# Kernel tuning notes

Hardware: AMD Instinct MI355X
Metric: run time of the kernel (lower is better)

The kernel has to match this reference:

```python
import jax, jax.numpy as jnp
import numpy as np

D_MODEL = 512
N_HEADS = 8
D_K = D_MODEL // N_HEADS


def setup_inputs() -> dict:
    key = jax.random.key(0)
    ks = jax.random.split(key, 12)
    B, S = 2, 4096
    std = 1.0 / np.sqrt(D_MODEL)
    inp = {
        "q": jax.random.normal(ks[0], (B, S, D_MODEL), jnp.float32),
        "k": jax.random.normal(ks[1], (B, S, D_MODEL), jnp.float32),
        "v": jax.random.normal(ks[2], (B, S, D_MODEL), jnp.float32),
        "Wq": jax.random.normal(ks[3], (D_MODEL, D_MODEL), jnp.float32) * std,
        "bq": jnp.zeros((D_MODEL,), jnp.float32),
        "Wk": jax.random.normal(ks[4], (D_MODEL, D_MODEL), jnp.float32) * std,
        "bk": jnp.zeros((D_MODEL,), jnp.float32),
        "Wv": jax.random.normal(ks[5], (D_MODEL, D_MODEL), jnp.float32) * std,
        "bv": jnp.zeros((D_MODEL,), jnp.float32),
        "Wo": jax.random.normal(ks[6], (D_MODEL, D_MODEL), jnp.float32) * std,
        "bo": jnp.zeros((D_MODEL,), jnp.float32),
        # torch init: ones
        "time_decay": jnp.ones((1, N_HEADS, 1, 1), jnp.float32) * 0.01,
        "scale": jnp.ones((1,), jnp.float32),
    }
    return inp


def reference(q, k, v, Wq, bq, Wk, bk, Wv, bv, Wo, bo, time_decay, scale):
    B, S, _ = q.shape
    # projections (torch Linear: x @ W.T + b), reshape to [B, H, S, d_k]
    def proj(x, W, b):
        y = x @ W.T + b
        return y.reshape(B, -1, N_HEADS, D_K).transpose(0, 2, 1, 3)

    qh = proj(q, Wq, bq)
    kh = proj(k, Wk, bk)
    vh = proj(v, Wv, bv)

    # scores: [B, H, Sq, Sk]
    scores = jnp.einsum("bhqd,bhkd->bhqk", qh, kh) / np.sqrt(D_K)
    scores = scores * scale
    # exponential decay over absolute key position (per-head learnable rate)
    pos = jnp.arange(S, dtype=scores.dtype)  # key positions
    decay = jnp.exp(-time_decay * jnp.abs(pos)[None, None, None, :])  # [1,H,1,Sk]
    scores = scores * decay

    attn = jax.nn.softmax(scores, axis=-1)
    context = jnp.einsum("bhqk,bhkd->bhqd", attn, vh)
    context = context.transpose(0, 2, 1, 3).reshape(B, S, D_MODEL)
    out = context @ Wo.T + bo
    return out
```

## Files before the change

kernel.cpp:

```cpp
#include <hip/hip_runtime.h>
#include <hip/hip_bf16.h>
#include <stdint.h>

typedef __attribute__((ext_vector_type(8))) __bf16 bf16x8;
typedef __attribute__((ext_vector_type(4))) float f32x4;
typedef __attribute__((ext_vector_type(16))) float f32x16;
typedef __attribute__((ext_vector_type(8))) unsigned short ushort8;
typedef __attribute__((ext_vector_type(4))) unsigned short ushort4v;
typedef __attribute__((ext_vector_type(2))) unsigned int uint2v;
typedef __attribute__((ext_vector_type(4))) unsigned int uint4v;

__device__ __forceinline__ unsigned short bfbits(float x) {
    __bf16 b = (__bf16)x;
    return __builtin_bit_cast(unsigned short, b);
}
__device__ __forceinline__ float bf2f_u(unsigned short u) {
    return __builtin_bit_cast(float, (unsigned int)u << 16);
}

__device__ __forceinline__ f32x4 mfma16(bf16x8 a, bf16x8 b, f32x4 c) {
    return __builtin_amdgcn_mfma_f32_16x16x32_bf16(a, b, c, 0, 0, 0);
}
__device__ __forceinline__ f32x16 mfma32(bf16x8 a, bf16x8 b, f32x16 c) {
    return __builtin_amdgcn_mfma_f32_32x32x16_bf16(a, b, c, 0, 0, 0);
}

__device__ __forceinline__ unsigned int cvtpk(float lo, float hi) {
    unsigned int r;
    asm("v_cvt_pk_bf16_f32 %0, %1, %2" : "=v"(r) : "v"(lo), "v"(hi));
    return r;
}

__device__ __forceinline__ float lanepull(float src, int srcl) {
    return __builtin_bit_cast(float,
        __builtin_amdgcn_ds_bpermute(srcl * 4, __builtin_bit_cast(int, src)));
}

__device__ __forceinline__ void gload16(const void* g, void* l) {
    __builtin_amdgcn_global_load_lds(
        (const __attribute__((address_space(1))) unsigned int*)g,
        (__attribute__((address_space(3))) unsigned int*)l, 16, 0, 0);
}

__device__ __forceinline__ f32x16 zero16() {
    f32x16 r;
    #pragma unroll
    for (int i = 0; i < 16; i++) r[i] = 0.f;
    return r;
}

__device__ __forceinline__ int tail_tiles(float tdh, float scale) {
    float cut = 5.3f + __logf(fmaxf(scale, 1e-20f));
    cut = fmaxf(cut, 0.f);
    tdh = fmaxf(tdh, 1e-8f);
    int kt = (int)ceilf(cut / (tdh * 64.f));
    if (kt < 1) kt = 1;
    if (kt > 64) kt = 64;
    return kt;
}

__global__ __launch_bounds__(256) void wconv(
    const float* __restrict__ Wq, const float* __restrict__ Wk,
    const float* __restrict__ Wv, const float* __restrict__ Wo,
    unsigned short* __restrict__ Wbf)
{
    const int t    = blockIdx.x * 256 + threadIdx.x;
    const int slab = t >> 15;
    const int off8 = t & 32767;
    const float* src = (slab == 0) ? Wq : (slab == 1) ? Wk : (slab == 2) ? Wv : Wo;
    float4 a = ((const float4*)(src + off8 * 8))[0];
    float4 b = ((const float4*)(src + off8 * 8))[1];
    uint4v pk = { cvtpk(a.x, a.y), cvtpk(a.z, a.w), cvtpk(b.x, b.y), cvtpk(b.z, b.w) };
    *(uint4v*)(Wbf + (size_t)slab * 262144 + off8 * 8) = pk;
}

__global__ __launch_bounds__(256) void gemm_qkv(
    const float* __restrict__ q, const float* __restrict__ k, const float* __restrict__ v,
    const unsigned short* __restrict__ Wbf,
    const float* __restrict__ bq, const float* __restrict__ bk, const float* __restrict__ bv,
    const float* __restrict__ td, const float* __restrict__ sc,
    unsigned short* __restrict__ Qh, unsigned short* __restrict__ Kh,
    unsigned short* __restrict__ Vt)
{
    __shared__ __align__(16) char ALDS[2][16384];

    const int id  = blockIdx.x;
    const int nid = (id & 7) * 96 + (id >> 3);
    const int z   = nid >> 8;
    const int rem = nid & 255;
    const int bm  = rem >> 2;
    const int bn  = rem & 3;

    const float* A0   = (z == 0) ? q  : (z == 1) ? k  : v;
    const float* bias = (z == 0) ? bq : (z == 1) ? bk : bv;

    const int tid  = threadIdx.x;
    const int lane = tid & 63;
    const int w    = tid >> 6;
    const int wm   = w >> 1, wn = w & 1;
    const int l15  = lane & 15;
    const int g    = lane >> 4;

    const int lr  = lane >> 3;
    const int lc  = ((lane & 7) * 16) ^ (lr << 4);
    const char* asrc[4];
    #pragma unroll
    for (int j = 0; j < 4; j++)
        asrc[j] = (const char*)A0 + (size_t)(bm * 128 + w * 32 + j * 8 + lr) * 2048 + lc;
    int adst[4];
    #pragma unroll
    for (int j = 0; j < 4; j++) adst[j] = w * 4096 + j * 1024;

    const unsigned short* Bp[4];
    #pragma unroll
    for (int n = 0; n < 4; n++)
        Bp[n] = Wbf + (size_t)z * 262144
              + (size_t)(bn * 128 + wn * 64 + n * 16 + l15) * 512 + g * 8;

    f32x4 acc[4][4];
    #pragma unroll
    for (int m = 0; m < 4; m++)
        #pragma unroll
        for (int n = 0; n < 4; n++)
            acc[m][n] = (f32x4){0.f, 0.f, 0.f, 0.f};

    const int arow = l15;
    const int asw  = (arow & 7) << 4;

    #pragma unroll
    for (int j = 0; j < 4; j++) gload16(asrc[j], ALDS[0] + adst[j]);
    bf16x8 BA[4], BB[4];
    #pragma unroll
    for (int n = 0; n < 4; n++) BA[n] = *(const bf16x8*)Bp[n];

#define QKV_ITER(CUR, KK, BC, BN)                                                  \
    {                                                                              \
        asm volatile("s_waitcnt vmcnt(0)" ::: "memory");                           \
        __syncthreads();                                                           \
        if ((KK) < 15) {                                                           \
            _Pragma("unroll")                                                      \
            for (int j = 0; j < 4; j++)                                            \
                gload16(asrc[j] + (size_t)((KK) + 1) * 128,                        \
                        ALDS[(CUR) ^ 1] + adst[j]);                                \
            _Pragma("unroll")                                                      \
            for (int n = 0; n < 4; n++)                                            \
                BN[n] = *(const bf16x8*)(Bp[n] + (size_t)((KK) + 1) * 32);         \
        }                                                                          \
        bf16x8 af[4];                                                              \
        _Pragma("unroll")                                                          \
        for (int m = 0; m < 4; m++) {                                              \
            const char* base = ALDS[CUR] + (wm * 64 + m * 16 + arow) * 128;        \
            f32x4 v0 = *(const f32x4*)(base + ((g * 32) ^ asw));                   \
            f32x4 v1 = *(const f32x4*)(base + (((g * 32) | 16) ^ asw));            \
            uint4v pk = { cvtpk(v0.x, v0.y), cvtpk(v0.z, v0.w),                    \
                          cvtpk(v1.x, v1.y), cvtpk(v1.z, v1.w) };                  \
            af[m] = __builtin_bit_cast(bf16x8, pk);                                \
        }                                                                          \
        __builtin_amdgcn_s_setprio(1);                                             \
        _Pragma("unroll")                                                          \
        for (int m = 0; m < 4; m++)                                                \
            _Pragma("unroll")                                                      \
            for (int n = 0; n < 4; n++)                                            \
                acc[m][n] = mfma16(af[m], BC[n], acc[m][n]);                       \
        __builtin_amdgcn_s_setprio(0);                                             \
    }

    #pragma unroll 1
    for (int t = 0; t < 8; ++t) {
        QKV_ITER(0, 2 * t, BA, BB)
        QKV_ITER(1, 2 * t + 1, BB, BA)
    }
#undef QKV_ITER

    const float coefL = sc[0] * 0.125f * 1.44269504f;

    #pragma unroll
    for (int m = 0; m < 4; m++) {
        const int grow0 = bm * 128 + wm * 64 + m * 16 + (g << 2);
        #pragma unroll
        for (int n = 0; n < 4; n++) {
            const int gcol = bn * 128 + wn * 64 + n * 16 + l15;
            const float bv2 = bias[gcol];
            f32x4 c = acc[m][n];
            const int b = grow0 >> 12, s0 = grow0 & 4095;
            const int h = gcol >> 6, dk = gcol & 63;
            if (z == 0) {
                const size_t base = ((size_t)(b * 8 + h) * 4096 + s0) * 64 + dk;
                #pragma unroll
                for (int r = 0; r < 4; r++)
                    Qh[base + (size_t)r * 64] = bfbits((c[r] + bv2) * coefL);
            } else if (z == 1) {
                const float tdh = td[h];
                const size_t base = ((size_t)(b * 8 + h) * 4096 + s0) * 64 + dk;
                #pragma unroll
                for (int r = 0; r < 4; r++)
                    Kh[base + (size_t)r * 64] = bfbits((c[r] + bv2) * __expf(-tdh * (float)(s0 + r)));
            } else {
                ushort4v pk = { bfbits(c[0] + bv2), bfbits(c[1] + bv2),
                                bfbits(c[2] + bv2), bfbits(c[3] + bv2) };
                *(ushort4v*)&Vt[((size_t)(b * 8 + h) * 64 + dk) * 4096 + s0] = pk;
            }
        }
    }
}

__global__ __launch_bounds__(256) void gemm_out(
    const unsigned short* __restrict__ Actx, const unsigned short* __restrict__ Wob,
    const float* __restrict__ bias, float* __restrict__ Out)
{
    __shared__ __align__(16) char ALDS[2][16384];

    const int id  = blockIdx.x;
    const int nid = (id & 7) * 64 + (id >> 3);
    const int bm  = nid >> 3;
    const int bn  = nid & 7;

    const int tid  = threadIdx.x;
    const int lane = tid & 63;
    const int w    = tid >> 6;
    const int wm   = w >> 1, wn = w & 1;
    const int l15  = lane & 15;
    const int g    = lane >> 4;

    const int lr  = lane >> 3;
    const int lc  = ((lane & 7) * 16) ^ (lr << 4);
    const char* asrc[4];
    #pragma unroll
    for (int j = 0; j < 4; j++)
        asrc[j] = (const char*)Actx + (size_t)(bm * 128 + w * 32 + j * 8 + lr) * 1024 + lc;
    int adst[4];
    #pragma unroll
    for (int j = 0; j < 4; j++) adst[j] = w * 4096 + j * 1024;

    const unsigned short* Bp[2];
    #pragma unroll
    for (int n = 0; n < 2; n++)
        Bp[n] = Wob + (size_t)(bn * 64 + wn * 32 + n * 16 + l15) * 512 + g * 8;

    f32x4 acc[4][2];
    #pragma unroll
    for (int m = 0; m < 4; m++)
        #pragma unroll
        for (int n = 0; n < 2; n++)
            acc[m][n] = (f32x4){0.f, 0.f, 0.f, 0.f};

    const int arow = l15;
    const int asw  = (arow & 7) << 4;

    #pragma unroll
    for (int j = 0; j < 4; j++) gload16(asrc[j], ALDS[0] + adst[j]);
    bf16x8 BA[2][2], BB[2][2];
    #pragma unroll
    for (int n = 0; n < 2; n++) {
        BA[n][0] = *(const bf16x8*)Bp[n];
        BA[n][1] = *(const bf16x8*)(Bp[n] + 32);
    }

#define OUT_ITER(CUR, KK, BC, BN)                                                  \
    {                                                                              \
        asm volatile("s_waitcnt vmcnt(0)" ::: "memory");                           \
        __syncthreads();                                                           \
        if ((KK) < 7) {                                                            \
            _Pragma("unroll")                                                      \
            for (int j = 0; j < 4; j++)                                            \
                gload16(asrc[j] + (size_t)((KK) + 1) * 128,                        \
                        ALDS[(CUR) ^ 1] + adst[j]);                                \
            _Pragma("unroll")                                                      \
            for (int n = 0; n < 2; n++) {                                          \
                BN[n][0] = *(const bf16x8*)(Bp[n] + (size_t)((KK) + 1) * 64);      \
                BN[n][1] = *(const bf16x8*)(Bp[n] + (size_t)((KK) + 1) * 64 + 32); \
            }                                                                      \
        }                                                                          \
        bf16x8 af[4][2];                                                           \
        _Pragma("unroll")                                                          \
        for (int m = 0; m < 4; m++) {                                              \
            const char* base = ALDS[CUR] + (wm * 64 + m * 16 + arow) * 128;        \
            af[m][0] = *(const bf16x8*)(base + ((g * 16) ^ asw));                  \
            af[m][1] = *(const bf16x8*)(base + ((64 + g * 16) ^ asw));             \
        }                                                                          \
        __builtin_amdgcn_s_setprio(1);                                             \
        _Pragma("unroll")                                                          \
        for (int m = 0; m < 4; m++)                                                \
            _Pragma("unroll")                                                      \
            for (int n = 0; n < 2; n++) {                                          \
                acc[m][n] = mfma16(af[m][0], BC[n][0], acc[m][n]);                 \
                acc[m][n] = mfma16(af[m][1], BC[n][1], acc[m][n]);                 \
            }                                                                      \
        __builtin_amdgcn_s_setprio(0);                                             \
    }

    #pragma unroll 1
    for (int t = 0; t < 4; ++t) {
        OUT_ITER(0, 2 * t, BA, BB)
        OUT_ITER(1, 2 * t + 1, BB, BA)
    }
#undef OUT_ITER

    #pragma unroll
    for (int m = 0; m < 4; m++) {
        const int grow0 = bm * 128 + wm * 64 + m * 16 + (g << 2);
        #pragma unroll
        for (int n = 0; n < 2; n++) {
            const int gcol = bn * 64 + wn * 32 + n * 16 + l15;
            const float bv2 = bias[gcol];
            f32x4 c = acc[m][n];
            #pragma unroll
            for (int r = 0; r < 4; r++)
                Out[(size_t)(grow0 + r) * 512 + gcol] = c[r] + bv2;
        }
    }
}

__global__ __launch_bounds__(512) void tail_pre(
    const unsigned short* __restrict__ Kh, const unsigned short* __restrict__ Vt,
    const float* __restrict__ td, const float* __restrict__ sc,
    unsigned short* __restrict__ Mt, float* __restrict__ SumV, float* __restrict__ KsL)
{
    __shared__ __align__(16) char KLDS[2][8192];
    __shared__ float redM[4][32][32];
    __shared__ float redv[64];
    __shared__ float redk[64];

    const int blk  = blockIdx.x;
    const int bh   = blk >> 3;
    const int part = blk & 7;
    const int h    = bh & 7;
    const int tid  = threadIdx.x;
    const int w    = tid >> 6;
    const int lane = tid & 63;
    const int l31  = lane & 31, hl = lane >> 5;
    const int d2q  = w & 1, d1q = (w >> 1) & 1, ksub = w >> 2;

    const int KT   = tail_tiles(td[h], sc[0]);
    const int K0   = KT * 64;
    const int nk   = 4096 - K0;
    const int q64  = nk >> 6;
    const int qb   = q64 >> 3, qr = q64 & 7;
    const int nch  = qb + (part < qr ? 1 : 0);
    const int ch0  = part * qb + (part < qr ? part : qr);
    const int kbeg = K0 + ch0 * 64;

    const int lr = lane >> 3;
    const int r8 = (w * 8 + lr) & 7;
    const char* ksrc = (const char*)Kh + (size_t)(bh * 4096 + kbeg + w * 8 + lr) * 128
                     + (((lane & 7) * 16) ^ (r8 << 4));
    const int kdst = w * 1024;

    const unsigned short* Vp = Vt + (size_t)(bh * 64 + d2q * 32 + l31) * 4096 + kbeg;

    f32x16 macc = zero16();
    float sumv = 0.f, ksum = 0.f;

    if (nch > 0) gload16(ksrc, KLDS[0] + kdst);

    #pragma unroll 1
    for (int ch = 0; ch < nch; ++ch) {
        asm volatile("s_waitcnt vmcnt(0)" ::: "memory");
        __syncthreads();
        if (ch + 1 < nch)
            gload16(ksrc + (size_t)(ch + 1) * 8192, KLDS[(ch + 1) & 1] + kdst);
        const char* kb = KLDS[ch & 1];

        #pragma unroll
        for (int mf = 0; mf < 2; mf++) {
            const int kloc0 = ksub * 32 + mf * 16 + hl * 8;
            ushort8 kbv;
            #pragma unroll
            for (int e = 0; e < 8; e++) {
                const int row = kloc0 + e;
                kbv[e] = *(const unsigned short*)(kb + row * 128
                          + ((d1q * 64 + l31 * 2) ^ ((row & 7) << 4)));
            }
            if (d2q == 0) {
                #pragma unroll
                for (int e = 0; e < 8; e++) ksum += bf2f_u(kbv[e]);
            }
            bf16x8 av = *(const bf16x8*)(Vp + ch * 64 + kloc0);
            if (d1q == 0) {
                ushort8 au = __builtin_bit_cast(ushort8, av);
                #pragma unroll
                for (int e = 0; e < 8; e++) sumv += bf2f_u(au[e]);
            }
            macc = mfma32(av, __builtin_bit_cast(bf16x8, kbv), macc);
        }
    }

    sumv += __shfl_xor(sumv, 32);
    ksum += __shfl_xor(ksum, 32);

    const int quad = d2q * 2 + d1q;
    __syncthreads();
    if (ksub == 0) {
        #pragma unroll
        for (int r = 0; r < 16; r++) {
            const int row = (r & 3) + 8 * (r >> 2) + 4 * hl;
            redM[quad][row][l31] = macc[r];
        }
        if (d1q == 0 && hl == 0) redv[d2q * 32 + l31] = sumv;
        if (d2q == 0 && hl == 0) redk[d1q * 32 + l31] = ksum;
    }
    __syncthreads();
    if (ksub == 1) {
        unsigned short* Mb = Mt + (size_t)part * 16 * 4096 + (size_t)bh * 4096;
        #pragma unroll
        for (int r = 0; r < 16; r++) {
            const int row = (r & 3) + 8 * (r >> 2) + 4 * hl;
            const float mv = (macc[r] + redM[quad][row][l31]) * 0.6931472f;
            Mb[(size_t)(d2q * 32 + row) * 64 + d1q * 32 + l31] = bfbits(mv);
        }
        if (d1q == 0 && hl == 0)
            SumV[part * 1024 + bh * 64 + d2q * 32 + l31] = sumv + redv[d2q * 32 + l31];
        if (d2q == 0 && hl == 0)
            KsL[part * 1024 + bh * 64 + d1q * 32 + l31] = (ksum + redk[d1q * 32 + l31]) * 0.6931472f;
    }
}

__global__ __launch_bounds__(256, 4) void attn_decay(
    const unsigned short* __restrict__ Qh, const unsigned short* __restrict__ Kh,
    const unsigned short* __restrict__ Vt, const float* __restrict__ td,
    const float* __restrict__ sc,
    const unsigned short* __restrict__ Mt, const float* __restrict__ SumV,
    const float* __restrict__ KsL, unsigned short* __restrict__ ctx)
{
    __shared__ __align__(16) char LDSB[32768];

    const int tid  = threadIdx.x;
    const int lane = tid & 63;
    const int w    = tid >> 6;
    const int qg   = w >> 1;
    const int ws   = w & 1;
    const int l31  = lane & 31;
    const int hl   = lane >> 5;

    const int i  = blockIdx.x;
    const int bh = ((i & 7) << 1) | ((i >> 9) & 1);
    const int qt = (i >> 3) & 63;
    const int h  = bh & 7;
    const int b  = bh >> 3;

    const int KT = tail_tiles(td[h], sc[0]);
    const int nk = 4096 - KT * 64;

    bf16x8 qf[4];
    {
        const unsigned short* Qp =
            Qh + ((size_t)bh * 4096 + qt * 64 + qg * 32 + l31) * 64 + hl * 8;
        #pragma unroll
        for (int c = 0; c < 4; c++)
            qf[c] = *(const bf16x8*)(Qp + c * 16);
    }

    f32x16 o0 = zero16(), o1 = zero16();
    float lp = 0.f;

    const char* kgp0; const char* kgp1; const char* vgp0; const char* vgp1;
    int ldsoff0, ldsoff1;
    {
        const size_t kbaseB = (size_t)bh * 4096 * 64 * 2;
        const size_t vbaseB = (size_t)bh * 64 * 4096 * 2;
        const int p0 = w * 2048 + lane * 16;
        const int r0 = p0 >> 7, c0 = p0 & 127, sw0 = (r0 & 7) << 4;
        const int p1 = w * 2048 + 1024 + lane * 16;
        const int r1 = p1 >> 7, c1 = p1 & 127, sw1 = (r1 & 7) << 4;
        kgp0 = (const char*)Kh + kbaseB + (size_t)r0 * 128  + (c0 ^ sw0);
        kgp1 = (const char*)Kh + kbaseB + (size_t)r1 * 128  + (c1 ^ sw1);
        vgp0 = (const char*)Vt + vbaseB + (size_t)r0 * 8192 + (c0 ^ sw0);
        vgp1 = (const char*)Vt + vbaseB + (size_t)r1 * 8192 + (c1 ^ sw1);
        ldsoff0 = w * 2048;
        ldsoff1 = w * 2048 + 1024;
    }
    gload16(kgp0, LDSB + ldsoff0);
    gload16(kgp1, LDSB + ldsoff1);
    gload16(vgp0, LDSB + 16384 + ldsoff0);
    gload16(vgp1, LDSB + 16384 + ldsoff1);
    kgp0 += 8192; kgp1 += 8192; vgp0 += 128; vgp1 += 128;

    const int krow = ws * 32 + l31;
    const int ksw  = (krow & 7) << 4;

#define ATTN_TILE(CUR, KT_IDX)                                                    \
    {                                                                             \
        asm volatile("s_waitcnt vmcnt(0)" ::: "memory");                          \
        __syncthreads();                                                          \
        if ((KT_IDX) + 1 < KT) {                                                  \
            gload16(kgp0, LDSB + ((CUR) ^ 1) * 8192 + ldsoff0);                   \
            gload16(kgp1, LDSB + ((CUR) ^ 1) * 8192 + ldsoff1);                   \
            gload16(vgp0, LDSB + 16384 + ((CUR) ^ 1) * 8192 + ldsoff0);           \
            gload16(vgp1, LDSB + 16384 + ((CUR) ^ 1) * 8192 + ldsoff1);           \
            kgp0 += 8192; kgp1 += 8192; vgp0 += 128; vgp1 += 128;                 \
        }                                                                         \
        const char* kb = LDSB + (CUR) * 8192;                                     \
        const char* vb = LDSB + 16384 + (CUR) * 8192;                             \
        f32x16 s = zero16();                                                      \
        __builtin_amdgcn_s_setprio(1);                                            \
        _Pragma("unroll")                                                         \
        for (int c = 0; c < 4; c++) {                                             \
            bf16x8 kf = *(const bf16x8*)(kb + krow * 128 + ((c * 32 + hl * 16) ^ ksw)); \
            s = mfma32(kf, qf[c], s);                                             \
        }                                                                         \
        __builtin_amdgcn_s_setprio(0);                                            \
        float p[16];                                                              \
        _Pragma("unroll")                                                         \
        for (int r = 0; r < 16; r++) {                                            \
            p[r] = __builtin_amdgcn_exp2f(s[r]);                                  \
            lp += p[r];                                                           \
        }                                                                         \
        unsigned int W0 = cvtpk(p[0], p[1]),   W1 = cvtpk(p[2], p[3]);            \
        unsigned int W2 = cvtpk(p[4], p[5]),   W3 = cvtpk(p[6], p[7]);            \
        unsigned int W4 = cvtpk(p[8], p[9]),   W5 = cvtpk(p[10], p[11]);          \
        unsigned int W6 = cvtpk(p[12], p[13]), W7 = cvtpk(p[14], p[15]);          \
        uint2v r02 = __builtin_amdgcn_permlane32_swap(W0, W2, false, false);      \
        uint2v r13 = __builtin_amdgcn_permlane32_swap(W1, W3, false, false);      \
        uint2v r46 = __builtin_amdgcn_permlane32_swap(W4, W6, false, false);      \
        uint2v r57 = __builtin_amdgcn_permlane32_swap(W5, W7, false, false);      \
        bf16x8 pa0 = __builtin_bit_cast(bf16x8, (uint4v){r02.x, r13.x, r02.y, r13.y}); \
        bf16x8 pa1 = __builtin_bit_cast(bf16x8, (uint4v){r46.x, r57.x, r46.y, r57.y}); \
        __builtin_amdgcn_s_setprio(1);                                            \
        {                                                                         \
            const int vr0  = l31;                                                 \
            const int vsw0 = (vr0 & 7) << 4;                                      \
            bf16x8 va = *(const bf16x8*)(vb + vr0 * 128 + ((ws * 64 + hl * 16) ^ vsw0));      \
            bf16x8 vb2 = *(const bf16x8*)(vb + vr0 * 128 + ((ws * 64 + 32 + hl * 16) ^ vsw0));\
            o0 = mfma32(pa0, va, o0);                                             \
            o0 = mfma32(pa1, vb2, o0);                                            \
            const int vr1  = 32 + l31;                                            \
            const int vsw1 = (vr1 & 7) << 4;                                      \
            bf16x8 vc = *(const bf16x8*)(vb + vr1 * 128 + ((ws * 64 + hl * 16) ^ vsw1));      \
            bf16x8 vd = *(const bf16x8*)(vb + vr1 * 128 + ((ws * 64 + 32 + hl * 16) ^ vsw1)); \
            o1 = mfma32(pa0, vc, o1);                                             \
            o1 = mfma32(pa1, vd, o1);                                             \
        }                                                                         \
        __builtin_amdgcn_s_setprio(0);                                            \
    }

    const int KT2 = KT >> 1;
    #pragma unroll 1
    for (int t = 0; t < KT2; ++t) {
        ATTN_TILE(0, 2 * t)
        ATTN_TILE(1, 2 * t + 1)
    }
    if (KT & 1) {
        ATTN_TILE(0, KT - 1)
    }
#undef ATTN_TILE

    if (ws == 0 && nk > 0) {
        float qk = 0.f;
        #pragma unroll
        for (int c = 0; c < 4; c++) {
            ushort8 qb2 = __builtin_bit_cast(ushort8, qf[c]);
            #pragma unroll
            for (int e = 0; e < 8; e++) {
                const int idx = c * 16 + hl * 8 + e;
                float ks = 0.f;
                #pragma unroll
                for (int part = 0; part < 8; part++)
                    ks += KsL[part * 1024 + bh * 64 + idx];
                qk += bf2f_u(qb2[e]) * ks;
            }
        }
        qk += __shfl_xor(qk, 32);
        if (hl == 0) lp += (float)nk + qk;

        #pragma unroll 1
        for (int part = 0; part < 8; part++) {
            const unsigned short* Mb = Mt + (size_t)part * 16 * 4096 + (size_t)bh * 4096;
            #pragma unroll
            for (int c = 0; c < 4; c++) {
                bf16x8 m0 = *(const bf16x8*)(Mb + (size_t)l31 * 64 + c * 16 + hl * 8);
                bf16x8 m1 = *(const bf16x8*)(Mb + (size_t)(32 + l31) * 64 + c * 16 + hl * 8);
                o0 = mfma32(qf[c], m0, o0);
                o1 = mfma32(qf[c], m1, o1);
            }
        }
        float sv0 = 0.f, sv1 = 0.f;
        #pragma unroll
        for (int part = 0; part < 8; part++) {
            sv0 += SumV[part * 1024 + bh * 64 + l31];
            sv1 += SumV[part * 1024 + bh * 64 + 32 + l31];
        }
        #pragma unroll
        for (int r = 0; r < 16; r++) { o0[r] += sv0; o1[r] += sv1; }
    }

    float lw = lp + __shfl_xor(lp, 32);
    __syncthreads();
    float* lscr = (float*)(LDSB + 16384);
    if (lane < 32)
        lscr[(qg * 2 + ws) * 32 + lane] = lw;
    __syncthreads();
    const float pl2 = lscr[(qg * 2 + (ws ^ 1)) * 32 + l31];
    const float myscale = 1.f / (lw + pl2);
    #pragma unroll
    for (int rc = 0; rc < 4; rc++)
        #pragma unroll
        for (int j = 0; j < 4; j++) {
            const float a = lanepull(myscale, rc * 8 + hl * 4 + j);
            o0[rc * 4 + j] *= a;
            o1[rc * 4 + j] *= a;
        }
    __syncthreads();
    float* Oscr = (float*)(LDSB + qg * 8192);
    if (ws == 1) {
        #pragma unroll
        for (int reg = 0; reg < 16; reg++) {
            const int row = (reg & 3) + 8 * (reg >> 2) + 4 * hl;
            Oscr[row * 64 + l31]      = o0[reg];
            Oscr[row * 64 + 32 + l31] = o1[reg];
        }
    }
    __syncthreads();
    if (ws == 0) {
        #pragma unroll
        for (int reg = 0; reg < 16; reg++) {
            const int row = (reg & 3) + 8 * (reg >> 2) + 4 * hl;
            const float v0 = o0[reg] + Oscr[row * 64 + l31];
            const float v1 = o1[reg] + Oscr[row * 64 + 32 + l31];
            const int srow_ = qt * 64 + qg * 32 + row;
            const size_t idx = ((size_t)b * 4096 + srow_) * 512 + h * 64;
            ctx[idx + l31]      = bfbits(v0);
            ctx[idx + 32 + l31] = bfbits(v1);
        }
    }
}

extern "C" void kernel_launch(void* const* d_in, const int* in_sizes, int n_in,
                              void* d_out, int out_size, void* d_ws, size_t ws_size,
                              hipStream_t stream)
{
    (void)in_sizes; (void)n_in; (void)out_size; (void)ws_size;
    const float* q  = (const float*)d_in[0];
    const float* k  = (const float*)d_in[1];
    const float* v  = (const float*)d_in[2];
    const float* Wq = (const float*)d_in[3];
    const float* bq = (const float*)d_in[4];
    const float* Wk = (const float*)d_in[5];
    const float* bk = (const float*)d_in[6];
    const float* Wv = (const float*)d_in[7];
    const float* bv = (const float*)d_in[8];
    const float* Wo = (const float*)d_in[9];
    const float* bo = (const float*)d_in[10];
    const float* td = (const float*)d_in[11];
    const float* sc = (const float*)d_in[12];

    unsigned short* Qh  = (unsigned short*)d_ws;
    unsigned short* Kh  = Qh + (size_t)16 * 4096 * 64;
    unsigned short* Vt  = Kh + (size_t)16 * 4096 * 64;
    unsigned short* ctx = Vt + (size_t)16 * 4096 * 64;
    unsigned short* Wbf = ctx + (size_t)16 * 4096 * 64;

    unsigned short* Mt   = (unsigned short*)d_out;
    float*          SumV = (float*)((char*)d_out + 8 * 16 * 4096 * 2);
    float*          KsL  = SumV + 8 * 1024;

    wconv<<<dim3(512), 256, 0, stream>>>(Wq, Wk, Wv, Wo, Wbf);
    gemm_qkv<<<dim3(768), 256, 0, stream>>>(q, k, v, Wbf, bq, bk, bv, td, sc, Qh, Kh, Vt);
    tail_pre<<<dim3(128), 512, 0, stream>>>(Kh, Vt, td, sc, Mt, SumV, KsL);
    attn_decay<<<dim3(1024), 256, 0, stream>>>(Qh, Kh, Vt, td, sc, Mt, SumV, KsL, ctx);
    gemm_out<<<dim3(512), 256, 0, stream>>>(ctx, Wbf + (size_t)3 * 262144, bo, (float*)d_out);
}
```

Baseline: 115.9 us.

## Triple-buffer QKV GEMM loads with partial vmcnt waits

The QKV projection GEMM moves from double to triple buffering of the A tile in LDS and B fragments in registers, prefetching two k-steps ahead. It waits with vmcnt(8) instead of draining all outstanding loads, and the loop is fully unrolled. This aims to hide global load latency behind MFMA work. The cost is 48KB of LDS, which may lower occupancy, plus more register pressure. Correctness depends on the vmcnt count matching the number of loads in flight.

Measured after the change: 114.0 us. Within noise of the previous version (-1.7%).

```diff
diff --git a/kernel.cpp b/kernel.cpp
--- a/kernel.cpp
+++ b/kernel.cpp
@@ -82,7 +82,7 @@
     unsigned short* __restrict__ Qh, unsigned short* __restrict__ Kh,
     unsigned short* __restrict__ Vt)
 {
-    __shared__ __align__(16) char ALDS[2][16384];
+    __shared__ __align__(16) char ALDS[3][16384];
 
     const int id  = blockIdx.x;
     const int nid = (id & 7) * 96 + (id >> 3);
@@ -127,29 +127,36 @@
     const int arow = l15;
     const int asw  = (arow & 7) << 4;
 
+    bf16x8 B0[4], B1[4], B2[4];
+
     #pragma unroll
     for (int j = 0; j < 4; j++) gload16(asrc[j], ALDS[0] + adst[j]);
-    bf16x8 BA[4], BB[4];
-    #pragma unroll
-    for (int n = 0; n < 4; n++) BA[n] = *(const bf16x8*)Bp[n];
-
-#define QKV_ITER(CUR, KK, BC, BN)                                                  \
+    #pragma unroll
+    for (int n = 0; n < 4; n++) B0[n] = *(const bf16x8*)Bp[n];
+    #pragma unroll
+    for (int j = 0; j < 4; j++) gload16(asrc[j] + 128, ALDS[1] + adst[j]);
+    #pragma unroll
+    for (int n = 0; n < 4; n++) B1[n] = *(const bf16x8*)(Bp[n] + 32);
+
+#define QKV_ITER(KK, BC, BN)                                                       \
     {                                                                              \
-        asm volatile("s_waitcnt vmcnt(0)" ::: "memory");                           \
-        __syncthreads();                                                           \
-        if ((KK) < 15) {                                                           \
+        if ((KK) == 15) { asm volatile("s_waitcnt vmcnt(0)" ::: "memory"); }       \
+        else            { asm volatile("s_waitcnt vmcnt(8)" ::: "memory"); }       \
+        __builtin_amdgcn_s_barrier();                                              \
+        __builtin_amdgcn_sched_barrier(0);                                         \
+        if ((KK) + 2 < 16) {                                                       \
             _Pragma("unroll")                                                      \
             for (int j = 0; j < 4; j++)                                            \
-                gload16(asrc[j] + (size_t)((KK) + 1) * 128,                        \
-                        ALDS[(CUR) ^ 1] + adst[j]);                                \
+                gload16(asrc[j] + (size_t)((KK) + 2) * 128,                        \
+                        ALDS[((KK) + 2) % 3] + adst[j]);                           \
             _Pragma("unroll")                                                      \
             for (int n = 0; n < 4; n++)                                            \
-                BN[n] = *(const bf16x8*)(Bp[n] + (size_t)((KK) + 1) * 32);         \
+                BN[n] = *(const bf16x8*)(Bp[n] + (size_t)((KK) + 2) * 32);         \
         }                                                                          \
         bf16x8 af[4];                                                              \
         _Pragma("unroll")                                                          \
         for (int m = 0; m < 4; m++) {                                              \
-            const char* base = ALDS[CUR] + (wm * 64 + m * 16 + arow) * 128;        \
+            const char* base = ALDS[(KK) % 3] + (wm * 64 + m * 16 + arow) * 128;   \
             f32x4 v0 = *(const f32x4*)(base + ((g * 32) ^ asw));                   \
             f32x4 v1 = *(const f32x4*)(base + (((g * 32) | 16) ^ asw));            \
             uint4v pk = { cvtpk(v0.x, v0.y), cvtpk(v0.z, v0.w),                    \
@@ -165,11 +172,12 @@
         __builtin_amdgcn_s_setprio(0);                                             \
     }
 
-    #pragma unroll 1
-    for (int t = 0; t < 8; ++t) {
-        QKV_ITER(0, 2 * t, BA, BB)
-        QKV_ITER(1, 2 * t + 1, BB, BA)
-    }
+    QKV_ITER(0,  B0, B2)  QKV_ITER(1,  B1, B0)  QKV_ITER(2,  B2, B1)
+    QKV_ITER(3,  B0, B2)  QKV_ITER(4,  B1, B0)  QKV_ITER(5,  B2, B1)
+    QKV_ITER(6,  B0, B2)  QKV_ITER(7,  B1, B0)  QKV_ITER(8,  B2, B1)
+    QKV_ITER(9,  B0, B2)  QKV_ITER(10, B1, B0)  QKV_ITER(11, B2, B1)
+    QKV_ITER(12, B0, B2)  QKV_ITER(13, B1, B0)  QKV_ITER(14, B2, B1)
+    QKV_ITER(15, B0, B2)
 #undef QKV_ITER
 
     const float coefL = sc[0] * 0.125f * 1.44269504f;
```
